# Performance work log

Hardware: AMD Instinct MI355X
Metric: run time of the kernel (lower is better)

The kernel has to match this reference:

```python
import jax, jax.numpy as jnp
import numpy as np

N = 200000
E = 1000000
IN_DIM = 16
HID = 64
OUT = 1
EPS = 1e-5


def setup_inputs() -> dict:
    key = jax.random.key(0)
    ks = jax.random.split(key, 24)
    x = jax.random.normal(ks[0], (N, IN_DIM), dtype=jnp.float32)
    edge_index = jax.random.randint(ks[1], (2, E), 0, N, dtype=jnp.int64)

    def lin(k, fan_in, fan_out):
        s = 1.0 / np.sqrt(fan_in)
        return jax.random.uniform(k, (fan_in, fan_out), jnp.float32, -s, s)

    inp = {
        'x': x, 'edge_index': edge_index,
        'W1': lin(ks[2], IN_DIM, HID), 'b1': jnp.zeros((HID,), jnp.float32),
        'W2': lin(ks[3], HID, HID), 'b2': jnp.zeros((HID,), jnp.float32),
        'W3': lin(ks[4], HID, HID), 'b3': jnp.zeros((HID,), jnp.float32),
        'fc_w': lin(ks[5], HID, OUT),
        'fc_b': jnp.zeros((OUT,), jnp.float32),
    }
    # BatchNorm params / running stats (eval mode) — randomized for nontrivial math
    for i, kk in zip((1, 2, 3), range(6, 24, 4)):
        inp[f'g{i}'] = 1.0 + 0.1 * jax.random.normal(ks[kk], (HID,), jnp.float32)
        inp[f'be{i}'] = 0.1 * jax.random.normal(ks[kk + 1], (HID,), jnp.float32)
        inp[f'm{i}'] = 0.1 * jax.random.normal(ks[kk + 2], (HID,), jnp.float32)
        inp[f'v{i}'] = 0.5 + jax.random.uniform(ks[kk + 3], (HID,), jnp.float32)
    return inp


def gcn_conv(x, src, dst, W, b):
    # PyG GCNConv: add self-loops, symmetric normalization, aggregate at dst, bias after aggregation
    h = x @ W                                   # [N, F]
    deg = 1.0 + jax.ops.segment_sum(jnp.ones((E,), x.dtype), dst, num_segments=N)
    dinv = jax.lax.rsqrt(deg)                   # deg >= 1 (self loop)
    norm = dinv[src] * dinv[dst]                # [E]
    msg = h[src] * norm[:, None]                # [E, F] gather + scale
    agg = jax.ops.segment_sum(msg, dst, num_segments=N)
    agg = agg + h * (dinv * dinv)[:, None]      # self-loop contribution
    return agg + b


def bn(x, g, be, m, v):
    return g * (x - m) * jax.lax.rsqrt(v + EPS) + be


def reference(x, edge_index, W1, b1, W2, b2, W3, b3, fc_w, fc_b,
              g1, be1, m1, v1, g2, be2, m2, v2, g3, be3, m3, v3):
    src, dst = edge_index[0], edge_index[1]
    h = jax.nn.relu(bn(gcn_conv(x, src, dst, W1, b1), g1, be1, m1, v1))
    residual = h  # dropout is identity in eval mode
    h = jax.nn.relu(bn(gcn_conv(h, src, dst, W2, b2), g2, be2, m2, v2))
    h = jax.nn.relu(bn(gcn_conv(h, src, dst, W3, b3), g3, be3, m3, v3))
    h = h + residual
    out = h @ fc_w + fc_b
    return jax.nn.sigmoid(out) * 10.0
```

## Files before the change

### kernel.cpp

```cpp
#include <hip/hip_runtime.h>
#include <hip/hip_bf16.h>
#include <math.h>

constexpr int HIDF = 64;

typedef __attribute__((ext_vector_type(8))) short short8;
typedef __attribute__((ext_vector_type(4))) float f32x4;

static inline size_t align_up(size_t x, size_t a) { return (x + a - 1) & ~(a - 1); }

__device__ inline ushort f2bf(float x) {
    __hip_bfloat16 h = __float2bfloat16(x);
    return __builtin_bit_cast(ushort, h);
}
__device__ inline float bf2f(ushort u) {
    return __builtin_bit_cast(float, (unsigned int)u << 16);
}
__device__ inline float bflo(unsigned int u) {
    return __builtin_bit_cast(float, u << 16);
}
__device__ inline float bfhi(unsigned int u) {
    return __builtin_bit_cast(float, u & 0xffff0000u);
}
__device__ inline unsigned int pack2(float lo, float hi) {
    return (unsigned int)f2bf(lo) | ((unsigned int)f2bf(hi) << 16);
}


__global__ __launch_bounds__(256) void k_hist(const int* __restrict__ dst,
                                              int* __restrict__ bukcnt,
                                              int ne, int nbuk) {
    __shared__ int lh[512];
    int tid = threadIdx.x;
    lh[tid] = 0; lh[tid + 256] = 0;
    __syncthreads();
#pragma unroll
    for (int k = 0; k < 8; ++k) {
        int idx = blockIdx.x * 2048 + k * 256 + tid;
        if (idx < ne) atomicAdd(&lh[dst[idx] >> 9], 1);
    }
    __syncthreads();
    for (int b = tid; b < nbuk; b += 256) {
        int c = lh[b];
        if (c) atomicAdd(&bukcnt[b], c);
    }
}

__global__ __launch_bounds__(512) void k_bukscan(const int* __restrict__ bukcnt,
                                                 int* __restrict__ bukbase,
                                                 int* __restrict__ gcur,
                                                 int* __restrict__ rowptr,
                                                 int nbuk, int ne, int n) {
    __shared__ int s[512];
    int tid = threadIdx.x;
    int c = (tid < nbuk) ? bukcnt[tid] : 0;
    s[tid] = c;
    __syncthreads();
    for (int off = 1; off < 512; off <<= 1) {
        int t = (tid >= off) ? s[tid - off] : 0;
        __syncthreads();
        s[tid] += t;
        __syncthreads();
    }
    int excl = s[tid] - c;
    if (tid < nbuk) { bukbase[tid] = excl; gcur[tid * 16] = excl; }
    if (tid == 0) { bukbase[nbuk] = ne; rowptr[n] = ne; }
}

__global__ __launch_bounds__(256) void k_scatter_pairs(
    const int* __restrict__ src, const int* __restrict__ dst,
    int* __restrict__ gcur, uint2* __restrict__ pairs, int ne, int nbuk) {
    __shared__ int lh[512];
    __shared__ int lb[512];
    int tid = threadIdx.x;
    int d[16], sv[16];
#pragma unroll
    for (int k = 0; k < 16; ++k) {
        int idx = blockIdx.x * 4096 + k * 256 + tid;
        bool ok = idx < ne;
        d[k] = ok ? dst[idx] : -1;
        sv[k] = ok ? src[idx] : 0;
    }
    lh[tid] = 0; lh[tid + 256] = 0;
    __syncthreads();
#pragma unroll
    for (int k = 0; k < 16; ++k)
        if (d[k] >= 0) atomicAdd(&lh[d[k] >> 9], 1);
    __syncthreads();
    for (int b = tid; b < nbuk; b += 256) {
        int c = lh[b];
        lb[b] = c ? atomicAdd(&gcur[b * 16], c) : 0;
    }
    __syncthreads();
#pragma unroll
    for (int k = 0; k < 16; ++k)
        if (d[k] >= 0) {
            int pos = atomicAdd(&lb[d[k] >> 9], 1);
            pairs[pos] = make_uint2((unsigned)sv[k], (unsigned)d[k]);
        }
}

__global__ __launch_bounds__(512) void k_bucket_sort(
    const uint2* __restrict__ pairs, const int* __restrict__ bukbase,
    int* __restrict__ rowptr, float* __restrict__ dinv,
    int* __restrict__ esrc, int n) {
    __shared__ int lcnt[512];
    __shared__ int lscan[512];
    __shared__ int lcur[512];
    __shared__ int stage[4096];
    int b = blockIdx.x, tid = threadIdx.x;
    int base = bukbase[b];
    int cnt = bukbase[b + 1] - base;
    lcnt[tid] = 0;
    __syncthreads();
    for (int i = tid; i < cnt; i += 512) {
        uint2 u = pairs[base + i];
        atomicAdd(&lcnt[u.y & 511], 1);
    }
    __syncthreads();
    int v = lcnt[tid];
    lscan[tid] = v;
    __syncthreads();
    for (int off = 1; off < 512; off <<= 1) {
        int t = (tid >= off) ? lscan[tid - off] : 0;
        __syncthreads();
        lscan[tid] += t;
        __syncthreads();
    }
    int excl = lscan[tid] - v;
    lcur[tid] = excl;
    int node = (b << 9) + tid;
    if (node < n) {
        rowptr[node] = base + excl;
        dinv[node] = rsqrtf(1.f + (float)v);
    }
    __syncthreads();
    for (int i = tid; i < cnt; i += 512) {
        uint2 u = pairs[base + i];
        int p = atomicAdd(&lcur[u.y & 511], 1);
        if (p < 4096) stage[p] = (int)u.x;
    }
    __syncthreads();
    for (int i = tid; i < cnt && i < 4096; i += 512)
        esrc[base + i] = stage[i];
}

__global__ __launch_bounds__(256) void k_prep(
    const float* __restrict__ W1, const float* __restrict__ W2,
    const float* __restrict__ W3, ushort* __restrict__ wb,
    const float* __restrict__ b1, const float* __restrict__ g1,
    const float* __restrict__ be1, const float* __restrict__ m1, const float* __restrict__ v1,
    const float* __restrict__ b2, const float* __restrict__ g2,
    const float* __restrict__ be2, const float* __restrict__ m2, const float* __restrict__ v2,
    const float* __restrict__ b3, const float* __restrict__ g3,
    const float* __restrict__ be3, const float* __restrict__ m3, const float* __restrict__ v3,
    float* __restrict__ ST) {
    int i = blockIdx.x * 256 + threadIdx.x;
    if (i < 1024) wb[i] = f2bf(W1[i]);
    else if (i < 5120) wb[i] = f2bf(W2[i - 1024]);
    else if (i < 9216) wb[i] = f2bf(W3[i - 5120]);
    int j = i - 9216;
    if (j >= 0 && j < 192) {
        int li = j >> 6, f = j & 63;
        const float* g  = li == 0 ? g1  : li == 1 ? g2  : g3;
        const float* be = li == 0 ? be1 : li == 1 ? be2 : be3;
        const float* m  = li == 0 ? m1  : li == 1 ? m2  : m3;
        const float* v  = li == 0 ? v1  : li == 1 ? v2  : v3;
        const float* bb = li == 0 ? b1  : li == 1 ? b2  : b3;
        float sc = g[f] * rsqrtf(v[f] + 1e-5f);
        ST[li * 128 + f] = sc;
        ST[li * 128 + 64 + f] = sc * (bb[f] - m[f]) + be[f];
    }
}

template <int K, bool F32IN>
__global__ __launch_bounds__(256) void k_gemm_mfma(
    const void* __restrict__ Av, const ushort* __restrict__ Wb,
    const float* __restrict__ dinv, ushort* __restrict__ hsb, int n) {
    constexpr int KT = (K >= 32) ? K / 32 : 1;
    int wid = (blockIdx.x * 256 + threadIdx.x) >> 6;
    int lane = threadIdx.x & 63;
    int lr = lane & 15, lg = lane >> 4;
    int row16 = wid * 16;
    if (row16 >= n) return;

    short8 bf[4][KT];
#pragma unroll
    for (int nt = 0; nt < 4; ++nt)
#pragma unroll
        for (int kt = 0; kt < KT; ++kt) {
            short8 f = {0, 0, 0, 0, 0, 0, 0, 0};
#pragma unroll
            for (int i = 0; i < 8; ++i) {
                int k = kt * 32 + lg * 8 + i;
                if (k < K) f[i] = (short)Wb[k * 64 + nt * 16 + lr];
            }
            bf[nt][kt] = f;
        }

    short8 af[KT];
#pragma unroll
    for (int kt = 0; kt < KT; ++kt) {
        short8 f = {0, 0, 0, 0, 0, 0, 0, 0};
        if (F32IN) {
            if (lg < 2) {
                const float* ar = (const float*)Av + (size_t)(row16 + lr) * K + lg * 8;
                float4 u0 = *reinterpret_cast<const float4*>(ar);
                float4 u1 = *reinterpret_cast<const float4*>(ar + 4);
                f[0] = (short)f2bf(u0.x); f[1] = (short)f2bf(u0.y);
                f[2] = (short)f2bf(u0.z); f[3] = (short)f2bf(u0.w);
                f[4] = (short)f2bf(u1.x); f[5] = (short)f2bf(u1.y);
                f[6] = (short)f2bf(u1.z); f[7] = (short)f2bf(u1.w);
            }
        } else {
            const ushort* A = (const ushort*)Av;
            if (K == 16) {
                if (lg < 2)
                    f = *reinterpret_cast<const short8*>(A + (size_t)(row16 + lr) * K + lg * 8);
            } else {
                f = *reinterpret_cast<const short8*>(A + (size_t)(row16 + lr) * K + kt * 32 + lg * 8);
            }
        }
        af[kt] = f;
    }

    f32x4 acc[4] = {{0, 0, 0, 0}, {0, 0, 0, 0}, {0, 0, 0, 0}, {0, 0, 0, 0}};
#pragma unroll
    for (int kt = 0; kt < KT; ++kt)
#pragma unroll
        for (int nt = 0; nt < 4; ++nt)
            acc[nt] = __builtin_amdgcn_mfma_f32_16x16x32_bf16(af[kt], bf[nt][kt], acc[nt], 0, 0, 0);

#pragma unroll
    for (int j = 0; j < 4; ++j) {
        int row = row16 + lg * 4 + j;
        float di = dinv[row];
#pragma unroll
        for (int nt = 0; nt < 4; ++nt)
            hsb[(size_t)row * 64 + nt * 16 + lr] = f2bf(acc[nt][j] * di);
    }
}

__device__ inline void addrow(float a[8], uint4 u) {
    a[0] += bflo(u.x); a[1] += bfhi(u.x);
    a[2] += bflo(u.y); a[3] += bfhi(u.y);
    a[4] += bflo(u.z); a[5] += bfhi(u.z);
    a[6] += bflo(u.w); a[7] += bfhi(u.w);
}

__global__ __launch_bounds__(256) void k_agg_epi(
    const ushort* __restrict__ hsb, const int* __restrict__ rowptr,
    const int* __restrict__ esrc, const float* __restrict__ dinv,
    const float* __restrict__ S, const float* __restrict__ T,
    ushort* __restrict__ hout, int n) {
    int t = blockIdx.x * 256 + threadIdx.x;
    int node = t >> 3;
    if (node >= n) return;
    int q = t & 7, lane = threadIdx.x & 63;
    const uint4* hs4 = reinterpret_cast<const uint4*>(hsb);
    float a[8] = {0, 0, 0, 0, 0, 0, 0, 0};
    addrow(a, hs4[(size_t)node * 8 + q]);
    int start = rowptr[node], deg = rowptr[node + 1] - start;
    int ev = (q < deg) ? esrc[start + q] : 0;
    int it = 0;
    for (; it + 2 <= deg; it += 2) {
        int s0 = (it < 8) ? __shfl(ev, (lane & 56) + it, 64) : esrc[start + it];
        int s1 = (it + 1 < 8) ? __shfl(ev, (lane & 56) + it + 1, 64) : esrc[start + it + 1];
        uint4 r0 = hs4[(size_t)s0 * 8 + q];
        uint4 r1 = hs4[(size_t)s1 * 8 + q];
        addrow(a, r0);
        addrow(a, r1);
    }
    if (it < deg) {
        int s0 = (it < 8) ? __shfl(ev, (lane & 56) + it, 64) : esrc[start + it];
        addrow(a, hs4[(size_t)s0 * 8 + q]);
    }
    float di = dinv[node];
    const float4* S4 = reinterpret_cast<const float4*>(S);
    const float4* T4 = reinterpret_cast<const float4*>(T);
    float4 sA = S4[q * 2], sB = S4[q * 2 + 1];
    float4 tA = T4[q * 2], tB = T4[q * 2 + 1];
    float o0 = fmaxf(fmaf(sA.x * di, a[0], tA.x), 0.f);
    float o1 = fmaxf(fmaf(sA.y * di, a[1], tA.y), 0.f);
    float o2 = fmaxf(fmaf(sA.z * di, a[2], tA.z), 0.f);
    float o3 = fmaxf(fmaf(sA.w * di, a[3], tA.w), 0.f);
    float o4 = fmaxf(fmaf(sB.x * di, a[4], tB.x), 0.f);
    float o5 = fmaxf(fmaf(sB.y * di, a[5], tB.y), 0.f);
    float o6 = fmaxf(fmaf(sB.z * di, a[6], tB.z), 0.f);
    float o7 = fmaxf(fmaf(sB.w * di, a[7], tB.w), 0.f);
    uint4 w;
    w.x = pack2(o0, o1); w.y = pack2(o2, o3);
    w.z = pack2(o4, o5); w.w = pack2(o6, o7);
    reinterpret_cast<uint4*>(hout)[(size_t)node * 8 + q] = w;
}

__global__ __launch_bounds__(256) void k_agg_final(
    const ushort* __restrict__ hsb, const int* __restrict__ rowptr,
    const int* __restrict__ esrc, const float* __restrict__ dinv,
    const float* __restrict__ S, const float* __restrict__ T,
    const ushort* __restrict__ h1, const float* __restrict__ fcw,
    const float* __restrict__ fcb, float* __restrict__ out, int n) {
    int t = blockIdx.x * 256 + threadIdx.x;
    int node = t >> 3;
    if (node >= n) return;
    int q = t & 7, lane = threadIdx.x & 63;
    const uint4* hs4 = reinterpret_cast<const uint4*>(hsb);
    float a[8] = {0, 0, 0, 0, 0, 0, 0, 0};
    addrow(a, hs4[(size_t)node * 8 + q]);
    int start = rowptr[node], deg = rowptr[node + 1] - start;
    int ev = (q < deg) ? esrc[start + q] : 0;
    int it = 0;
    for (; it + 2 <= deg; it += 2) {
        int s0 = (it < 8) ? __shfl(ev, (lane & 56) + it, 64) : esrc[start + it];
        int s1 = (it + 1 < 8) ? __shfl(ev, (lane & 56) + it + 1, 64) : esrc[start + it + 1];
        uint4 r0 = hs4[(size_t)s0 * 8 + q];
        uint4 r1 = hs4[(size_t)s1 * 8 + q];
        addrow(a, r0);
        addrow(a, r1);
    }
    if (it < deg) {
        int s0 = (it < 8) ? __shfl(ev, (lane & 56) + it, 64) : esrc[start + it];
        addrow(a, hs4[(size_t)s0 * 8 + q]);
    }
    float di = dinv[node];
    const float4* S4 = reinterpret_cast<const float4*>(S);
    const float4* T4 = reinterpret_cast<const float4*>(T);
    float4 sA = S4[q * 2], sB = S4[q * 2 + 1];
    float4 tA = T4[q * 2], tB = T4[q * 2 + 1];
    uint4 r = reinterpret_cast<const uint4*>(h1)[(size_t)node * 8 + q];
    float h0 = fmaxf(fmaf(sA.x * di, a[0], tA.x), 0.f) + bflo(r.x);
    float h1v = fmaxf(fmaf(sA.y * di, a[1], tA.y), 0.f) + bfhi(r.x);
    float h2 = fmaxf(fmaf(sA.z * di, a[2], tA.z), 0.f) + bflo(r.y);
    float h3 = fmaxf(fmaf(sA.w * di, a[3], tA.w), 0.f) + bfhi(r.y);
    float h4 = fmaxf(fmaf(sB.x * di, a[4], tB.x), 0.f) + bflo(r.z);
    float h5 = fmaxf(fmaf(sB.y * di, a[5], tB.y), 0.f) + bfhi(r.z);
    float h6 = fmaxf(fmaf(sB.z * di, a[6], tB.z), 0.f) + bflo(r.w);
    float h7 = fmaxf(fmaf(sB.w * di, a[7], tB.w), 0.f) + bfhi(r.w);
    float4 fA = reinterpret_cast<const float4*>(fcw)[q * 2];
    float4 fB = reinterpret_cast<const float4*>(fcw)[q * 2 + 1];
    float p = h0 * fA.x + h1v * fA.y + h2 * fA.z + h3 * fA.w +
              h4 * fB.x + h5 * fB.y + h6 * fB.z + h7 * fB.w;
    p += __shfl_xor(p, 1, 64);
    p += __shfl_xor(p, 2, 64);
    p += __shfl_xor(p, 4, 64);
    if (q == 0) out[node] = 10.f / (1.f + expf(-(p + fcb[0])));
}

extern "C" void kernel_launch(void* const* d_in, const int* in_sizes, int n_in,
                              void* d_out, int out_size, void* d_ws, size_t ws_size,
                              hipStream_t stream) {
    const float* x   = (const float*)d_in[0];
    const int*   ei  = (const int*)d_in[1];
    const float* W1  = (const float*)d_in[2];
    const float* b1  = (const float*)d_in[3];
    const float* W2  = (const float*)d_in[4];
    const float* b2  = (const float*)d_in[5];
    const float* W3  = (const float*)d_in[6];
    const float* b3  = (const float*)d_in[7];
    const float* fcw = (const float*)d_in[8];
    const float* fcb = (const float*)d_in[9];
    const float* g1 = (const float*)d_in[10], *be1 = (const float*)d_in[11];
    const float* m1 = (const float*)d_in[12], *v1  = (const float*)d_in[13];
    const float* g2 = (const float*)d_in[14], *be2 = (const float*)d_in[15];
    const float* m2 = (const float*)d_in[16], *v2  = (const float*)d_in[17];
    const float* g3 = (const float*)d_in[18], *be3 = (const float*)d_in[19];
    const float* m3 = (const float*)d_in[20], *v3  = (const float*)d_in[21];

    const int N = in_sizes[0] / 16;
    const int E = in_sizes[1] / 2;
    const int* src = ei;
    const int* dst = ei + E;
    float* out = (float*)d_out;

    char* w = (char*)d_ws;
    auto take = [&](size_t bytes) { char* p = w; w += align_up(bytes, 256); return p; };
    float*  dinv    = (float*)take((size_t)N * 4);
    int*    rowptr  = (int*)take((size_t)(N + 1) * 4);
    int*    bukcnt  = (int*)take(512 * 4);
    int*    bukbase = (int*)take(513 * 4);
    int*    gcur    = (int*)take(512 * 16 * 4);
    uint2*  pairs   = (uint2*)take((size_t)E * 8);
    int*    esrc    = (int*)take((size_t)E * 4);
    ushort* hsb     = (ushort*)take((size_t)N * HIDF * 2);
    ushort* h1b     = (ushort*)take((size_t)N * HIDF * 2);
    ushort* h2b     = (ushort*)take((size_t)N * HIDF * 2);
    ushort* wb      = (ushort*)take((size_t)9216 * 2);
    float*  ST      = (float*)take(3 * 128 * 4);

    const int NBUK  = (N + 511) >> 9;
    const int gHist = (E + 2047) / 2048;
    const int gScat = (E + 4095) / 4096;
    const int gT    = ((N + 15) / 16 * 64 + 255) / 256;
    const int gAgg  = (N * 8 + 255) / 256;

    hipMemsetAsync(bukcnt, 0, 512 * 4, stream);
    k_hist<<<gHist, 256, 0, stream>>>(dst, bukcnt, E, NBUK);
    k_bukscan<<<1, 512, 0, stream>>>(bukcnt, bukbase, gcur, rowptr, NBUK, E, N);
    k_scatter_pairs<<<gScat, 256, 0, stream>>>(src, dst, gcur, pairs, E, NBUK);
    k_bucket_sort<<<NBUK, 512, 0, stream>>>(pairs, bukbase, rowptr, dinv, esrc, N);

    k_prep<<<37, 256, 0, stream>>>(W1, W2, W3, wb,
                                   b1, g1, be1, m1, v1,
                                   b2, g2, be2, m2, v2,
                                   b3, g3, be3, m3, v3, ST);

    k_gemm_mfma<16, true><<<gT, 256, 0, stream>>>(x, wb, dinv, hsb, N);
    k_agg_epi<<<gAgg, 256, 0, stream>>>(hsb, rowptr, esrc, dinv,
                                        ST, ST + 64, h1b, N);
    k_gemm_mfma<64, false><<<gT, 256, 0, stream>>>(h1b, wb + 1024, dinv, hsb, N);
    k_agg_epi<<<gAgg, 256, 0, stream>>>(hsb, rowptr, esrc, dinv,
                                        ST + 128, ST + 192, h2b, N);
    k_gemm_mfma<64, false><<<gT, 256, 0, stream>>>(h2b, wb + 5120, dinv, hsb, N);
    k_agg_final<<<gAgg, 256, 0, stream>>>(hsb, rowptr, esrc, dinv,
                                          ST + 256, ST + 320, h1b, fcw, fcb, out, N);
}
```

Before: 268.8 us.

## Fuse aggregation epilogue with next-layer GEMM and pack sort pairs into 32 bits

The aggregation-plus-BN/ReLU epilogue is fused with the following layer's 64x64 MFMA GEMM. Each block aggregates 32 nodes, stages the bf16 rows in shared memory, and multiplies them by W, so the intermediate h2 activation is never written to or read back from global memory. Two separate GEMM launches are removed, and the write of the layer-1 activation is kept only because it serves as the residual. Sort pairs are packed as an 18-bit source plus a 9-bit local destination in one 32-bit word, halving the pair traffic in the CSR build. The gather loop is unrolled by four. The fused kernel reloads W from global memory in every block and may lower occupancy, and the packing assumes N stays below 2^18.

After: 255.0 us. 5.2% less time.

```diff
diff --git a/kernel.cpp b/kernel.cpp
--- a/kernel.cpp
+++ b/kernel.cpp
@@ -12,9 +12,6 @@
 __device__ inline ushort f2bf(float x) {
     __hip_bfloat16 h = __float2bfloat16(x);
     return __builtin_bit_cast(ushort, h);
-}
-__device__ inline float bf2f(ushort u) {
-    return __builtin_bit_cast(float, (unsigned int)u << 16);
 }
 __device__ inline float bflo(unsigned int u) {
     return __builtin_bit_cast(float, u << 16);
@@ -69,7 +66,7 @@
 
 __global__ __launch_bounds__(256) void k_scatter_pairs(
     const int* __restrict__ src, const int* __restrict__ dst,
-    int* __restrict__ gcur, uint2* __restrict__ pairs, int ne, int nbuk) {
+    int* __restrict__ gcur, unsigned* __restrict__ pairs, int ne, int nbuk) {
     __shared__ int lh[512];
     __shared__ int lb[512];
     int tid = threadIdx.x;
@@ -96,12 +93,12 @@
     for (int k = 0; k < 16; ++k)
         if (d[k] >= 0) {
             int pos = atomicAdd(&lb[d[k] >> 9], 1);
-            pairs[pos] = make_uint2((unsigned)sv[k], (unsigned)d[k]);
+            pairs[pos] = (unsigned)sv[k] | ((unsigned)(d[k] & 511) << 18);
         }
 }
 
 __global__ __launch_bounds__(512) void k_bucket_sort(
-    const uint2* __restrict__ pairs, const int* __restrict__ bukbase,
+    const unsigned* __restrict__ pairs, const int* __restrict__ bukbase,
     int* __restrict__ rowptr, float* __restrict__ dinv,
     int* __restrict__ esrc, int n) {
     __shared__ int lcnt[512];
@@ -113,10 +110,8 @@
     int cnt = bukbase[b + 1] - base;
     lcnt[tid] = 0;
     __syncthreads();
-    for (int i = tid; i < cnt; i += 512) {
-        uint2 u = pairs[base + i];
-        atomicAdd(&lcnt[u.y & 511], 1);
-    }
+    for (int i = tid; i < cnt; i += 512)
+        atomicAdd(&lcnt[pairs[base + i] >> 18], 1);
     __syncthreads();
     int v = lcnt[tid];
     lscan[tid] = v;
@@ -136,9 +131,9 @@
     }
     __syncthreads();
     for (int i = tid; i < cnt; i += 512) {
-        uint2 u = pairs[base + i];
-        int p = atomicAdd(&lcur[u.y & 511], 1);
-        if (p < 4096) stage[p] = (int)u.x;
+        unsigned u = pairs[base + i];
+        int p = atomicAdd(&lcur[u >> 18], 1);
+        if (p < 4096) stage[p] = (int)(u & 0x3FFFF);
     }
     __syncthreads();
     for (int i = tid; i < cnt && i < 4096; i += 512)
@@ -173,63 +168,41 @@
     }
 }
 
-template <int K, bool F32IN>
-__global__ __launch_bounds__(256) void k_gemm_mfma(
-    const void* __restrict__ Av, const ushort* __restrict__ Wb,
+__global__ __launch_bounds__(256) void k_gemm1(
+    const float* __restrict__ X, const ushort* __restrict__ Wb,
     const float* __restrict__ dinv, ushort* __restrict__ hsb, int n) {
-    constexpr int KT = (K >= 32) ? K / 32 : 1;
     int wid = (blockIdx.x * 256 + threadIdx.x) >> 6;
     int lane = threadIdx.x & 63;
     int lr = lane & 15, lg = lane >> 4;
     int row16 = wid * 16;
     if (row16 >= n) return;
 
-    short8 bf[4][KT];
+    short8 bf[4];
+#pragma unroll
+    for (int nt = 0; nt < 4; ++nt) {
+        short8 f = {0, 0, 0, 0, 0, 0, 0, 0};
+        if (lg < 2)
+#pragma unroll
+            for (int i = 0; i < 8; ++i)
+                f[i] = (short)Wb[(lg * 8 + i) * 64 + nt * 16 + lr];
+        bf[nt] = f;
+    }
+
+    short8 af = {0, 0, 0, 0, 0, 0, 0, 0};
+    if (lg < 2) {
+        const float* ar = X + (size_t)(row16 + lr) * 16 + lg * 8;
+        float4 u0 = *reinterpret_cast<const float4*>(ar);
+        float4 u1 = *reinterpret_cast<const float4*>(ar + 4);
+        af[0] = (short)f2bf(u0.x); af[1] = (short)f2bf(u0.y);
+        af[2] = (short)f2bf(u0.z); af[3] = (short)f2bf(u0.w);
+        af[4] = (short)f2bf(u1.x); af[5] = (short)f2bf(u1.y);
+        af[6] = (short)f2bf(u1.z); af[7] = (short)f2bf(u1.w);
+    }
+
+    f32x4 acc[4] = {{0, 0, 0, 0}, {0, 0, 0, 0}, {0, 0, 0, 0}, {0, 0, 0, 0}};
 #pragma unroll
     for (int nt = 0; nt < 4; ++nt)
-#pragma unroll
-        for (int kt = 0; kt < KT; ++kt) {
-            short8 f = {0, 0, 0, 0, 0, 0, 0, 0};
-#pragma unroll
-            for (int i = 0; i < 8; ++i) {
-                int k = kt * 32 + lg * 8 + i;
-                if (k < K) f[i] = (short)Wb[k * 64 + nt * 16 + lr];
-            }
-            bf[nt][kt] = f;
-        }
-
-    short8 af[KT];
-#pragma unroll
-    for (int kt = 0; kt < KT; ++kt) {
-        short8 f = {0, 0, 0, 0, 0, 0, 0, 0};
-        if (F32IN) {
-            if (lg < 2) {
-                const float* ar = (const float*)Av + (size_t)(row16 + lr) * K + lg * 8;
-                float4 u0 = *reinterpret_cast<const float4*>(ar);
-                float4 u1 = *reinterpret_cast<const float4*>(ar + 4);
-                f[0] = (short)f2bf(u0.x); f[1] = (short)f2bf(u0.y);
-                f[2] = (short)f2bf(u0.z); f[3] = (short)f2bf(u0.w);
-                f[4] = (short)f2bf(u1.x); f[5] = (short)f2bf(u1.y);
-                f[6] = (short)f2bf(u1.z); f[7] = (short)f2bf(u1.w);
-            }
-        } else {
-            const ushort* A = (const ushort*)Av;
-            if (K == 16) {
-                if (lg < 2)
-                    f = *reinterpret_cast<const short8*>(A + (size_t)(row16 + lr) * K + lg * 8);
-            } else {
-                f = *reinterpret_cast<const short8*>(A + (size_t)(row16 + lr) * K + kt * 32 + lg * 8);
-            }
-        }
-        af[kt] = f;
-    }
-
-    f32x4 acc[4] = {{0, 0, 0, 0}, {0, 0, 0, 0}, {0, 0, 0, 0}, {0, 0, 0, 0}};
-#pragma unroll
-    for (int kt = 0; kt < KT; ++kt)
-#pragma unroll
-        for (int nt = 0; nt < 4; ++nt)
-            acc[nt] = __builtin_amdgcn_mfma_f32_16x16x32_bf16(af[kt], bf[nt][kt], acc[nt], 0, 0, 0);
+        acc[nt] = __builtin_amdgcn_mfma_f32_16x16x32_bf16(af, bf[nt], acc[nt], 0, 0, 0);
 
 #pragma unroll
     for (int j = 0; j < 4; ++j) {
@@ -248,50 +221,109 @@
     a[6] += bflo(u.w); a[7] += bfhi(u.w);
 }
 
-__global__ __launch_bounds__(256) void k_agg_epi(
-    const ushort* __restrict__ hsb, const int* __restrict__ rowptr,
+__device__ inline void agg_core(const uint4* hs4, const int* rowptr,
+                                const int* esrc, int node, int q, int lane,
+                                float a[8]) {
+    addrow(a, hs4[(size_t)node * 8 + q]);
+    int start = rowptr[node], deg = rowptr[node + 1] - start;
+    int gb = lane & 56;
+    int ev = (q < deg) ? esrc[start + q] : 0;
+    int it = 0;
+    for (; it + 4 <= deg; it += 4) {
+        int s0 = (it + 0 < 8) ? __shfl(ev, gb + it + 0, 64) : esrc[start + it + 0];
+        int s1 = (it + 1 < 8) ? __shfl(ev, gb + it + 1, 64) : esrc[start + it + 1];
+        int s2 = (it + 2 < 8) ? __shfl(ev, gb + it + 2, 64) : esrc[start + it + 2];
+        int s3 = (it + 3 < 8) ? __shfl(ev, gb + it + 3, 64) : esrc[start + it + 3];
+        uint4 r0 = hs4[(size_t)s0 * 8 + q];
+        uint4 r1 = hs4[(size_t)s1 * 8 + q];
+        uint4 r2 = hs4[(size_t)s2 * 8 + q];
+        uint4 r3 = hs4[(size_t)s3 * 8 + q];
+        addrow(a, r0); addrow(a, r1); addrow(a, r2); addrow(a, r3);
+    }
+    for (; it < deg; ++it) {
+        int s = (it < 8) ? __shfl(ev, gb + it, 64) : esrc[start + it];
+        addrow(a, hs4[(size_t)s * 8 + q]);
+    }
+}
+
+template <bool WRITE_H>
+__global__ __launch_bounds__(256) void k_agg_gemm(
+    const ushort* __restrict__ hsbIn, const int* __restrict__ rowptr,
     const int* __restrict__ esrc, const float* __restrict__ dinv,
     const float* __restrict__ S, const float* __restrict__ T,
-    ushort* __restrict__ hout, int n) {
-    int t = blockIdx.x * 256 + threadIdx.x;
-    int node = t >> 3;
-    if (node >= n) return;
-    int q = t & 7, lane = threadIdx.x & 63;
-    const uint4* hs4 = reinterpret_cast<const uint4*>(hsb);
-    float a[8] = {0, 0, 0, 0, 0, 0, 0, 0};
-    addrow(a, hs4[(size_t)node * 8 + q]);
-    int start = rowptr[node], deg = rowptr[node + 1] - start;
-    int ev = (q < deg) ? esrc[start + q] : 0;
-    int it = 0;
-    for (; it + 2 <= deg; it += 2) {
-        int s0 = (it < 8) ? __shfl(ev, (lane & 56) + it, 64) : esrc[start + it];
-        int s1 = (it + 1 < 8) ? __shfl(ev, (lane & 56) + it + 1, 64) : esrc[start + it + 1];
-        uint4 r0 = hs4[(size_t)s0 * 8 + q];
-        uint4 r1 = hs4[(size_t)s1 * 8 + q];
-        addrow(a, r0);
-        addrow(a, r1);
-    }
-    if (it < deg) {
-        int s0 = (it < 8) ? __shfl(ev, (lane & 56) + it, 64) : esrc[start + it];
-        addrow(a, hs4[(size_t)s0 * 8 + q]);
-    }
-    float di = dinv[node];
-    const float4* S4 = reinterpret_cast<const float4*>(S);
-    const float4* T4 = reinterpret_cast<const float4*>(T);
-    float4 sA = S4[q * 2], sB = S4[q * 2 + 1];
-    float4 tA = T4[q * 2], tB = T4[q * 2 + 1];
-    float o0 = fmaxf(fmaf(sA.x * di, a[0], tA.x), 0.f);
-    float o1 = fmaxf(fmaf(sA.y * di, a[1], tA.y), 0.f);
-    float o2 = fmaxf(fmaf(sA.z * di, a[2], tA.z), 0.f);
-    float o3 = fmaxf(fmaf(sA.w * di, a[3], tA.w), 0.f);
-    float o4 = fmaxf(fmaf(sB.x * di, a[4], tB.x), 0.f);
-    float o5 = fmaxf(fmaf(sB.y * di, a[5], tB.y), 0.f);
-    float o6 = fmaxf(fmaf(sB.z * di, a[6], tB.z), 0.f);
-    float o7 = fmaxf(fmaf(sB.w * di, a[7], tB.w), 0.f);
-    uint4 w;
-    w.x = pack2(o0, o1); w.y = pack2(o2, o3);
-    w.z = pack2(o4, o5); w.w = pack2(o6, o7);
-    reinterpret_cast<uint4*>(hout)[(size_t)node * 8 + q] = w;
+    const ushort* __restrict__ Wb, ushort* __restrict__ hb_out,
+    ushort* __restrict__ hs_out, int n) {
+    __shared__ uint4 hl[8 * 32];
+    int tid = threadIdx.x;
+    int lane = tid & 63;
+    int node0 = blockIdx.x * 32;
+    int ln = tid >> 3;
+    int node = node0 + ln;
+    int q = tid & 7;
+
+    uint4 w = make_uint4(0u, 0u, 0u, 0u);
+    if (node < n) {
+        float a[8] = {0, 0, 0, 0, 0, 0, 0, 0};
+        agg_core(reinterpret_cast<const uint4*>(hsbIn), rowptr, esrc, node, q, lane, a);
+        float di = dinv[node];
+        const float4* S4 = reinterpret_cast<const float4*>(S);
+        const float4* T4 = reinterpret_cast<const float4*>(T);
+        float4 sA = S4[q * 2], sB = S4[q * 2 + 1];
+        float4 tA = T4[q * 2], tB = T4[q * 2 + 1];
+        float o0 = fmaxf(fmaf(sA.x * di, a[0], tA.x), 0.f);
+        float o1 = fmaxf(fmaf(sA.y * di, a[1], tA.y), 0.f);
+        float o2 = fmaxf(fmaf(sA.z * di, a[2], tA.z), 0.f);
+        float o3 = fmaxf(fmaf(sA.w * di, a[3], tA.w), 0.f);
+        float o4 = fmaxf(fmaf(sB.x * di, a[4], tB.x), 0.f);
+        float o5 = fmaxf(fmaf(sB.y * di, a[5], tB.y), 0.f);
+        float o6 = fmaxf(fmaf(sB.z * di, a[6], tB.z), 0.f);
+        float o7 = fmaxf(fmaf(sB.w * di, a[7], tB.w), 0.f);
+        w.x = pack2(o0, o1); w.y = pack2(o2, o3);
+        w.z = pack2(o4, o5); w.w = pack2(o6, o7);
+        if (WRITE_H)
+            reinterpret_cast<uint4*>(hb_out)[(size_t)node * 8 + q] = w;
+    }
+    hl[q * 32 + ln] = w;
+    __syncthreads();
+
+    int wv = tid >> 6;
+    int wr = wv >> 1, wc = wv & 1;
+    int lr = lane & 15, lg = lane >> 4;
+
+    short8 af[2];
+#pragma unroll
+    for (int kt = 0; kt < 2; ++kt)
+        af[kt] = __builtin_bit_cast(short8, hl[(kt * 4 + lg) * 32 + wr * 16 + lr]);
+
+    short8 bf[2][2];
+#pragma unroll
+    for (int nt = 0; nt < 2; ++nt)
+#pragma unroll
+        for (int kt = 0; kt < 2; ++kt) {
+            short8 f;
+#pragma unroll
+            for (int i = 0; i < 8; ++i)
+                f[i] = (short)Wb[(kt * 32 + lg * 8 + i) * 64 + wc * 32 + nt * 16 + lr];
+            bf[nt][kt] = f;
+        }
+
+    f32x4 acc[2] = {{0, 0, 0, 0}, {0, 0, 0, 0}};
+#pragma unroll
+    for (int kt = 0; kt < 2; ++kt)
+#pragma unroll
+        for (int nt = 0; nt < 2; ++nt)
+            acc[nt] = __builtin_amdgcn_mfma_f32_16x16x32_bf16(af[kt], bf[nt][kt], acc[nt], 0, 0, 0);
+
+#pragma unroll
+    for (int j = 0; j < 4; ++j) {
+        int row = node0 + wr * 16 + lg * 4 + j;
+        if (row < n) {
+            float di = dinv[row];
+#pragma unroll
+            for (int nt = 0; nt < 2; ++nt)
+                hs_out[(size_t)row * 64 + wc * 32 + nt * 16 + lr] = f2bf(acc[nt][j] * di);
+        }
+    }
 }
 
 __global__ __launch_bounds__(256) void k_agg_final(
@@ -304,24 +336,8 @@
     int node = t >> 3;
     if (node >= n) return;
     int q = t & 7, lane = threadIdx.x & 63;
-    const uint4* hs4 = reinterpret_cast<const uint4*>(hsb);
     float a[8] = {0, 0, 0, 0, 0, 0, 0, 0};
-    addrow(a, hs4[(size_t)node * 8 + q]);
-    int start = rowptr[node], deg = rowptr[node + 1] - start;
-    int ev = (q < deg) ? esrc[start + q] : 0;
-    int it = 0;
-    for (; it + 2 <= deg; it += 2) {
-        int s0 = (it < 8) ? __shfl(ev, (lane & 56) + it, 64) : esrc[start + it];
-        int s1 = (it + 1 < 8) ? __shfl(ev, (lane & 56) + it + 1, 64) : esrc[start + it + 1];
-        uint4 r0 = hs4[(size_t)s0 * 8 + q];
-        uint4 r1 = hs4[(size_t)s1 * 8 + q];
-        addrow(a, r0);
-        addrow(a, r1);
-    }
-    if (it < deg) {
-        int s0 = (it < 8) ? __shfl(ev, (lane & 56) + it, 64) : esrc[start + it];
-        addrow(a, hs4[(size_t)s0 * 8 + q]);
-    }
+    agg_core(reinterpret_cast<const uint4*>(hsb), rowptr, esrc, node, q, lane, a);
     float di = dinv[node];
     const float4* S4 = reinterpret_cast<const float4*>(S);
     const float4* T4 = reinterpret_cast<const float4*>(T);
@@ -374,23 +390,24 @@
 
     char* w = (char*)d_ws;
     auto take = [&](size_t bytes) { char* p = w; w += align_up(bytes, 256); return p; };
-    float*  dinv    = (float*)take((size_t)N * 4);
-    int*    rowptr  = (int*)take((size_t)(N + 1) * 4);
-    int*    bukcnt  = (int*)take(512 * 4);
-    int*    bukbase = (int*)take(513 * 4);
-    int*    gcur    = (int*)take(512 * 16 * 4);
-    uint2*  pairs   = (uint2*)take((size_t)E * 8);
-    int*    esrc    = (int*)take((size_t)E * 4);
-    ushort* hsb     = (ushort*)take((size_t)N * HIDF * 2);
-    ushort* h1b     = (ushort*)take((size_t)N * HIDF * 2);
-    ushort* h2b     = (ushort*)take((size_t)N * HIDF * 2);
-    ushort* wb      = (ushort*)take((size_t)9216 * 2);
-    float*  ST      = (float*)take(3 * 128 * 4);
+    float*    dinv    = (float*)take((size_t)N * 4);
+    int*      rowptr  = (int*)take((size_t)(N + 1) * 4);
+    int*      bukcnt  = (int*)take(512 * 4);
+    int*      bukbase = (int*)take(513 * 4);
+    int*      gcur    = (int*)take(512 * 16 * 4);
+    unsigned* pairs   = (unsigned*)take((size_t)E * 4);
+    int*      esrc    = (int*)take((size_t)E * 4);
+    ushort*   hsbA    = (ushort*)take((size_t)N * HIDF * 2);
+    ushort*   hsbB    = (ushort*)take((size_t)N * HIDF * 2);
+    ushort*   h1b     = (ushort*)take((size_t)N * HIDF * 2);
+    ushort*   wb      = (ushort*)take((size_t)9216 * 2);
+    float*    ST      = (float*)take(3 * 128 * 4);
 
     const int NBUK  = (N + 511) >> 9;
     const int gHist = (E + 2047) / 2048;
     const int gScat = (E + 4095) / 4096;
     const int gT    = ((N + 15) / 16 * 64 + 255) / 256;
+    const int gAG   = (N + 31) / 32;
     const int gAgg  = (N * 8 + 255) / 256;
 
     hipMemsetAsync(bukcnt, 0, 512 * 4, stream);
@@ -404,13 +421,11 @@
                                    b2, g2, be2, m2, v2,
                                    b3, g3, be3, m3, v3, ST);
 
-    k_gemm_mfma<16, true><<<gT, 256, 0, stream>>>(x, wb, dinv, hsb, N);
-    k_agg_epi<<<gAgg, 256, 0, stream>>>(hsb, rowptr, esrc, dinv,
-                                        ST, ST + 64, h1b, N);
-    k_gemm_mfma<64, false><<<gT, 256, 0, stream>>>(h1b, wb + 1024, dinv, hsb, N);
-    k_agg_epi<<<gAgg, 256, 0, stream>>>(hsb, rowptr, esrc, dinv,
-                                        ST + 128, ST + 192, h2b, N);
-    k_gemm_mfma<64, false><<<gT, 256, 0, stream>>>(h2b, wb + 5120, dinv, hsb, N);
-    k_agg_final<<<gAgg, 256, 0, stream>>>(hsb, rowptr, esrc, dinv,
+    k_gemm1<<<gT, 256, 0, stream>>>(x, wb, dinv, hsbA, N);
+    k_agg_gemm<true><<<gAG, 256, 0, stream>>>(hsbA, rowptr, esrc, dinv,
+                                              ST, ST + 64, wb + 1024, h1b, hsbB, N);
+    k_agg_gemm<false><<<gAG, 256, 0, stream>>>(hsbB, rowptr, esrc, dinv,
+                                               ST + 128, ST + 192, wb + 5120, nullptr, hsbA, N);
+    k_agg_final<<<gAgg, 256, 0, stream>>>(hsbA, rowptr, esrc, dinv,
                                           ST + 256, ST + 320, h1b, fcw, fcb, out, N);
 }
```
